# Optimization experiments

Measured on AMD Instinct MI355X. Metric: run time of the kernel, lower is better.

The kernel has to match this reference:

```python
import jax, jax.numpy as jnp
import numpy as np

BN_EPS = 1e-5
K = 3  # k_size


def _unfold(x, k):
    # torch F.unfold with padding=k//2, stride=1, viewed as (B, C, k*k, H, W).
    # Kernel positions are row-major (i slow, j fast), matching torch layout.
    p = k // 2
    B, C, H, W = x.shape
    xp = jnp.pad(x, ((0, 0), (0, 0), (p, p), (p, p)))
    pats = jnp.stack([xp[:, :, i:i + H, j:j + W]
                      for i in range(k) for j in range(k)], axis=2)
    return pats  # (B, C, k*k, H, W)


def _conv1x1(x, w, b):
    # w: (C_out, C_in), x: (B, C_in, H, W)
    return jnp.einsum('oc,bchw->bohw', w, x) + b[None, :, None, None]


def _bn(x, gamma, beta, mean, var):
    inv = gamma / jnp.sqrt(var + BN_EPS)
    return x * inv[None, :, None, None] + (beta - mean * inv)[None, :, None, None]


def setup_inputs() -> dict:
    key = jax.random.key(0)
    ks = jax.random.split(key, 12)
    B, C, H, W = 8, 256, 64, 64
    s = lambda k_, *sh: jax.random.normal(k_, sh, dtype=jnp.float32) * 0.05
    return {
        'x': jax.random.normal(ks[0], (B, C, H, W), dtype=jnp.float32),
        # feature_embedding: Conv2d(C, C, 1) + BN
        'w_embed': s(ks[1], C, C), 'b_embed': jnp.zeros((C,), jnp.float32),
        'bn1_gamma': jnp.ones((C,), jnp.float32), 'bn1_beta': jnp.zeros((C,), jnp.float32),
        'bn1_mean': jnp.zeros((C,), jnp.float32), 'bn1_var': jnp.ones((C,), jnp.float32),
        # enhance: Conv2d(2C, C, 1) + BN
        'w_enh': s(ks[2], C, 2 * C), 'b_enh': jnp.zeros((C,), jnp.float32),
        'bn2_gamma': jnp.ones((C,), jnp.float32), 'bn2_beta': jnp.zeros((C,), jnp.float32),
        'bn2_mean': jnp.zeros((C,), jnp.float32), 'bn2_var': jnp.ones((C,), jnp.float32),
        # weight_gen: Conv2d(2C, C//4, 1) -> ReLU -> Conv2d(C//4, C, 1) -> Sigmoid
        'w_g1': s(ks[3], C // 4, 2 * C), 'b_g1': jnp.zeros((C // 4,), jnp.float32),
        'w_g2': s(ks[4], C, C // 4), 'b_g2': jnp.zeros((C,), jnp.float32),
    }


def reference(x, w_embed, b_embed, bn1_gamma, bn1_beta, bn1_mean, bn1_var,
              w_enh, b_enh, bn2_gamma, bn2_beta, bn2_mean, bn2_var,
              w_g1, b_g1, w_g2, b_g2):
    B, C, H, W = x.shape
    # ---- feature embedding: 1x1 conv + BN (eval) + ReLU
    fe = jax.nn.relu(_bn(_conv1x1(x, w_embed, b_embed),
                         bn1_gamma, bn1_beta, bn1_mean, bn1_var))
    # ---- region similarity: cosine(center pixel, each kxk neighbor) over C
    pats = _unfold(fe, K)                       # (B, C, k2, H, W)
    sim = jnp.einsum('bchw,bckhw->bkhw', fe, pats)
    norm_c = jnp.sqrt(jnp.sum(fe * fe, axis=1))             # (B, H, W)
    norm_p = jnp.sqrt(jnp.sum(pats * pats, axis=1))         # (B, k2, H, W)
    sim = sim / (norm_c[:, None] * norm_p + 1e-7)
    sim = jax.nn.softmax(sim, axis=1)                       # over k2 window
    # ---- dynamic feature aggregation on original x
    xpats = _unfold(x, K)                                   # (B, C, k2, H, W)
    agg = jnp.einsum('bckhw,bkhw->bchw', xpats, sim)
    enhanced = jax.nn.relu(_bn(_conv1x1(jnp.concatenate([x, agg], axis=1), w_enh, b_enh),
                               bn2_gamma, bn2_beta, bn2_mean, bn2_var))
    # ---- output modulation (SE-style gating)
    pooled = jnp.mean(jnp.concatenate([x, enhanced], axis=1), axis=(2, 3), keepdims=True)
    h = jax.nn.relu(_conv1x1(pooled, w_g1, b_g1))
    weights = jax.nn.sigmoid(_conv1x1(h, w_g2, b_g2))       # (B, C, 1, 1)
    return x + weights * enhanced
```

## Files before the change

### kernel.cpp

```cpp
#include <hip/hip_runtime.h>
#include <math.h>

typedef unsigned short u16;
typedef unsigned int   u32;
typedef __attribute__((ext_vector_type(8))) short short8;
typedef __attribute__((ext_vector_type(4))) short s16x4;
typedef __attribute__((ext_vector_type(4))) float f32x4;

#define OFS_XB   0ul
#define OFS_W1B  8388608ul
#define OFS_W2B  8421376ul
#define OFS_B1   8486912ul
#define OFS_B2   8487168ul
#define OFS_POOL 8487424ul
#define OFS_ENH  8491520ul

__device__ __forceinline__ u16 f2bf(float x) {
    union { float f; u32 u; } v; v.f = x;
    u32 r = v.u + 0x7fffu + ((v.u >> 16) & 1u);
    return (u16)(r >> 16);
}
__device__ __forceinline__ float bf2f(u16 h) {
    union { u32 u; float f; } v; v.u = ((u32)h) << 16;
    return v.f;
}
__device__ __forceinline__ void ld_g2l_16(u16* l, const u16* g) {
    __builtin_amdgcn_global_load_lds(
        (const __attribute__((address_space(1))) u32*)g,
        (__attribute__((address_space(3))) u32*)l,
        16, 0, 0);
}

__global__ __launch_bounds__(256) void k_cvt(
    const float* __restrict__ x, u16* __restrict__ xb, float* __restrict__ pool,
    const float* __restrict__ w1, const float* __restrict__ b1,
    const float* __restrict__ g1, const float* __restrict__ be1,
    const float* __restrict__ m1, const float* __restrict__ v1,
    const float* __restrict__ w2, const float* __restrict__ b2,
    const float* __restrict__ g2, const float* __restrict__ be2,
    const float* __restrict__ m2, const float* __restrict__ v2,
    u16* __restrict__ w1b, u16* __restrict__ w2b,
    float* __restrict__ b1f, float* __restrict__ b2f)
{
    __shared__ float tile[64][65];
    const int t = threadIdx.x;
    const int id = blockIdx.x;
    if (id < 1) {
        const float4 z = {0.f, 0.f, 0.f, 0.f};
#pragma unroll
        for (int i = 0; i < 4; ++i) ((float4*)pool)[i * 256 + t] = z;
        return;
    }
    if (id < 771) {
        int idx = (id - 1) * 256 + t;
        if (idx < 65536) {
            int o = idx >> 8;
            float inv = g1[o] * rsqrtf(v1[o] + 1e-5f);
            w1b[idx] = f2bf(w1[idx] * inv);
        } else if (idx < 196608) {
            int j = idx - 65536;
            int o = j >> 9;
            float inv = g2[o] * rsqrtf(v2[o] + 1e-5f);
            w2b[j] = f2bf(w2[j] * inv);
        } else if (idx < 196864) {
            int o = idx - 196608;
            float inv = g1[o] * rsqrtf(v1[o] + 1e-5f);
            b1f[o] = b1[o] * inv + be1[o] - m1[o] * inv;
        } else if (idx < 197120) {
            int o = idx - 196864;
            float inv = g2[o] * rsqrtf(v2[o] + 1e-5f);
            b2f[o] = b2[o] * inv + be2[o] - m2[o] * inv;
        }
        return;
    }
    const int cid = id - 771;
    const int pt = cid & 63, ct = (cid >> 6) & 3, b = cid >> 8;
    const float* src = x + (((size_t)(b * 256 + ct * 64)) << 12) + pt * 64;
#pragma unroll
    for (int i = 0; i < 16; ++i) {
        int idx = i * 256 + t;
        int cl = idx >> 6, pl = idx & 63;
        tile[cl][pl] = src[((size_t)cl << 12) + pl];
    }
    __syncthreads();
#pragma unroll
    for (int i = 0; i < 8; ++i) {
        int idx = i * 256 + t;
        int pl = idx >> 5, c2 = idx & 31;
        int cl = c2 * 2;
        u32 lo = f2bf(tile[cl][pl]);
        u32 hi = f2bf(tile[cl + 1][pl]);
        *(u32*)(xb + (((size_t)(b * 4096 + pt * 64 + pl)) << 9) + ct * 64 + cl) = lo | (hi << 16);
    }
    if (t < 64) {
        float s = 0.f;
#pragma unroll
        for (int i = 0; i < 64; ++i) s += tile[t][i];
        atomicAdd(&pool[(b << 9) + ct * 64 + t], s * (1.f / 4096.f));
    }
}

template<int KIN, bool OUTT, bool DOPOOL>
__global__ __launch_bounds__(256) void k_gemm(
    const u16* __restrict__ xb, const u16* __restrict__ Wb,
    const float* __restrict__ biasf, void* __restrict__ outp,
    float* __restrict__ poolp)
{
    __shared__ __align__(16) u16 Wl[4096];
    __shared__ __align__(16) u16 Xl[4096];
    __shared__ __align__(16) u16 ct[OUTT ? 16384 : 4];
    __shared__ float sbias[128];
    const int t = threadIdx.x;
    const int lane = t & 63;
    const int wv = t >> 6;
    const int id = blockIdx.x;
    const int p_blk = (((id >> 4) << 3) | (id & 7)) * 128;
    const int o_blk = ((id >> 3) & 1) * 128;
    const int owg = (wv & 1) * 4;
    const int pwg = (wv >> 1) * 4;
    const int r16 = lane & 15, q = lane >> 4;
    if (t < 128) sbias[t] = biasf[o_blk + t];

    f32x4 acc[4][4];
#pragma unroll
    for (int i = 0; i < 4; ++i)
#pragma unroll
        for (int j = 0; j < 4; ++j) acc[i][j] = (f32x4){0.f, 0.f, 0.f, 0.f};

    for (int kc = 0; kc < KIN / 32; ++kc) {
        const int kk = kc * 32 + q * 8;
#pragma unroll
        for (int s = 0; s < 4; ++s) {
            const int bi = wv * 4 + s;
            const u16* g;
            u16* l;
            if (bi < 8) {
                g = Wb + (size_t)(o_blk + bi * 16 + r16) * KIN + kk;
                l = Wl + bi * 512;
            } else {
                g = xb + (((size_t)(p_blk + (bi - 8) * 16 + r16)) << 9) + kk;
                l = Xl + (bi - 8) * 512;
            }
            ld_g2l_16(l, g);
        }
        __syncthreads();
        short8 af[4], bf[4];
#pragma unroll
        for (int i = 0; i < 4; ++i) af[i] = *(const short8*)(Wl + (owg + i) * 512 + lane * 8);
#pragma unroll
        for (int j = 0; j < 4; ++j) bf[j] = *(const short8*)(Xl + (pwg + j) * 512 + lane * 8);
#pragma unroll
        for (int i = 0; i < 4; ++i)
#pragma unroll
            for (int j = 0; j < 4; ++j)
                acc[i][j] = __builtin_amdgcn_mfma_f32_16x16x32_bf16(af[i], bf[j], acc[i][j], 0, 0, 0);
        __syncthreads();
    }

    float bia[4][4];
#pragma unroll
    for (int i = 0; i < 4; ++i)
#pragma unroll
        for (int r = 0; r < 4; ++r) bia[i][r] = sbias[owg * 16 + i * 16 + q * 4 + r];
    const int bidx = p_blk >> 12;

    if (OUTT) {
#pragma unroll
        for (int i = 0; i < 4; ++i) {
#pragma unroll
            for (int j = 0; j < 4; ++j) {
                const int px_l = pwg * 16 + j * 16 + r16;
#pragma unroll
                for (int rp = 0; rp < 2; ++rp) {
                    const int r0 = rp * 2;
                    const int o_l = owg * 16 + i * 16 + q * 4 + r0;
                    const float v0 = fmaxf(acc[i][j][r0] + bia[i][r0], 0.f);
                    const float v1 = fmaxf(acc[i][j][r0 + 1] + bia[i][r0 + 1], 0.f);
                    const u32 pk = (u32)f2bf(v0) | ((u32)f2bf(v1) << 16);
                    *(u32*)((char*)ct + px_l * 256 + ((o_l * 2) ^ ((px_l & 7) << 4))) = pk;
                }
            }
        }
        __syncthreads();
        u16* feT = (u16*)outp;
#pragma unroll
        for (int it = 0; it < 16; ++it) {
            const int idx = it * 256 + t;
            const int px_l = idx >> 5, cd = idx & 31;
            s16x4 v = *(const s16x4*)((char*)ct + px_l * 256 + ((cd * 8) ^ ((px_l & 7) << 4)));
            *(s16x4*)(feT + (((size_t)(bidx * 4096 + (p_blk & 4095) + px_l)) << 8) + o_blk + cd * 4) = v;
        }
        return;
    }

    const int pin0 = (p_blk & 4095) + pwg * 16 + r16;
#pragma unroll
    for (int i = 0; i < 4; ++i) {
#pragma unroll
        for (int r = 0; r < 4; ++r) {
            const int o = o_blk + owg * 16 + i * 16 + q * 4 + r;
            const size_t rowb = ((size_t)(bidx * 256 + o)) << 12;
            float ps = 0.f;
#pragma unroll
            for (int j = 0; j < 4; ++j) {
                float v = fmaxf(acc[i][j][r] + bia[i][r], 0.f);
                const size_t oi = rowb + pin0 + j * 16;
                ((u16*)outp)[oi] = f2bf(v);
                ps += v;
            }
            if (DOPOOL) {
                ps += __shfl_down(ps, 8, 16);
                ps += __shfl_down(ps, 4, 16);
                ps += __shfl_down(ps, 2, 16);
                ps += __shfl_down(ps, 1, 16);
                if (r16 == 0)
                    atomicAdd(&poolp[(bidx << 9) + 256 + o], ps * (1.f / 4096.f));
            }
        }
    }
}

__global__ __launch_bounds__(512) void k_simagg(
    const u16* __restrict__ fe, const u16* __restrict__ xb, u16* __restrict__ xbo)
{
    __shared__ float red[8][64][13];
    __shared__ float ws9[9][64];
    const int t = threadIdx.x;
    const int id = blockIdx.x;
    const int b = id & 7, h = id >> 3;
    const int rows[3] = {h > 0 ? h - 1 : 0, h, h < 63 ? h + 1 : 63};
    const int w = t & 63, sl = t >> 6;

    {
        const int wl = w > 0 ? w - 1 : 0, wr = w < 63 ? w + 1 : 63;
        const int pxs[3] = {wl, w, wr};
        const u16* feb = fe + (((size_t)(b * 4096)) << 8) + sl * 32;
        float cvec[32];
        float dot[9];
        float nn0 = 0.f, nn2 = 0.f;
        {
            const u16* p = feb + (((size_t)(rows[1] * 64 + w)) << 8);
            float s = 0.f;
#pragma unroll
            for (int i = 0; i < 4; ++i) {
                short8 v = *(const short8*)(p + i * 8);
#pragma unroll
                for (int u = 0; u < 8; ++u) {
                    float f = bf2f((u16)v[u]);
                    cvec[i * 8 + u] = f;
                    s = fmaf(f, f, s);
                }
            }
            dot[4] = s;
        }
#pragma unroll
        for (int r = 0; r < 3; ++r) {
#pragma unroll
            for (int j = 0; j < 3; ++j) {
                if (r == 1 && j == 1) continue;
                const int k = r * 3 + j;
                const u16* p = feb + (((size_t)(rows[r] * 64 + pxs[j])) << 8);
                float s = 0.f, qq = 0.f;
#pragma unroll
                for (int i = 0; i < 4; ++i) {
                    short8 v = *(const short8*)(p + i * 8);
#pragma unroll
                    for (int u = 0; u < 8; ++u) {
                        float f = bf2f((u16)v[u]);
                        s = fmaf(cvec[i * 8 + u], f, s);
                        if (j == 1) qq = fmaf(f, f, qq);
                    }
                }
                dot[k] = s;
                if (j == 1) { if (r == 0) nn0 = qq; else nn2 = qq; }
            }
        }
#pragma unroll
        for (int k = 0; k < 9; ++k) red[sl][w][k] = dot[k];
        red[sl][w][9] = nn0;
        red[sl][w][10] = nn2;
    }
    __syncthreads();
    if (t < 64) {
        float dk[9];
#pragma unroll
        for (int k = 0; k < 9; ++k) {
            float s = red[0][w][k];
#pragma unroll
            for (int g = 1; g < 8; ++g) s += red[g][w][k];
            dk[k] = s;
        }
        float nr0 = red[0][w][9], nr2 = red[0][w][10];
#pragma unroll
        for (int g = 1; g < 8; ++g) { nr0 += red[g][w][9]; nr2 += red[g][w][10]; }
        float nr[3] = {nr0, dk[4], nr2};
        const float nc = sqrtf(dk[4]);
        float sv[9], mk[9];
#pragma unroll
        for (int di = -1; di <= 1; ++di) {
#pragma unroll
            for (int dj = -1; dj <= 1; ++dj) {
                const int k = (di + 1) * 3 + (dj + 1);
                const int hn = h + di, wn = w + dj;
                const float mask = (hn >= 0 && hn < 64 && wn >= 0 && wn < 64) ? 1.f : 0.f;
                const int wc = wn < 0 ? 0 : (wn > 63 ? 63 : wn);
                const float nk = __shfl(nr[di + 1], wc, 64);
                mk[k] = mask;
                sv[k] = mask * dk[k] / (nc * sqrtf(nk) + 1e-7f);
            }
        }
        float mx = sv[0];
#pragma unroll
        for (int k = 1; k < 9; ++k) mx = fmaxf(mx, sv[k]);
        float e[9], sum = 0.f;
#pragma unroll
        for (int k = 0; k < 9; ++k) { e[k] = expf(sv[k] - mx); sum += e[k]; }
        const float rs = 1.f / sum;
#pragma unroll
        for (int k = 0; k < 9; ++k) ws9[k][w] = mk[k] * e[k] * rs;
    }
    __syncthreads();
    const int cd = t & 63, pxg = t >> 6;
    const u16* xbb = xb + (((size_t)(b * 4096)) << 9) + cd * 4;
    u16* orow = xbo + (((size_t)(b * 4096 + h * 64)) << 9) + 256 + cd * 4;
#pragma unroll
    for (int pi = 0; pi < 8; ++pi) {
        const int px = pxg * 8 + pi;
        const int pL = px > 0 ? px - 1 : 0, pR = px < 63 ? px + 1 : 63;
        const int pxs2[3] = {pL, px, pR};
        float m9[9];
#pragma unroll
        for (int k = 0; k < 9; ++k) m9[k] = ws9[k][px];
        float a0 = 0.f, a1 = 0.f, a2 = 0.f, a3 = 0.f;
#pragma unroll
        for (int r = 0; r < 3; ++r) {
#pragma unroll
            for (int j = 0; j < 3; ++j) {
                const float m = m9[r * 3 + j];
                s16x4 v = *(const s16x4*)(xbb + (((size_t)(rows[r] * 64 + pxs2[j])) << 9));
                a0 = fmaf(bf2f((u16)v[0]), m, a0);
                a1 = fmaf(bf2f((u16)v[1]), m, a1);
                a2 = fmaf(bf2f((u16)v[2]), m, a2);
                a3 = fmaf(bf2f((u16)v[3]), m, a3);
            }
        }
        s16x4 sv4;
        sv4[0] = (short)f2bf(a0); sv4[1] = (short)f2bf(a1);
        sv4[2] = (short)f2bf(a2); sv4[3] = (short)f2bf(a3);
        *(s16x4*)(orow + ((size_t)px << 9)) = sv4;
    }
}

__global__ __launch_bounds__(256) void k_final(
    const float* __restrict__ x, const u16* __restrict__ enh,
    const float* __restrict__ pool,
    const float* __restrict__ wg1, const float* __restrict__ bg1,
    const float* __restrict__ wg2, const float* __restrict__ bg2,
    float* __restrict__ out)
{
    __shared__ float pl[512];
    __shared__ float hpart[4][64];
    __shared__ float hb[64];
    __shared__ float sg[256];
    const int t = threadIdx.x;
    const int id = blockIdx.x;
    const int b = id & 7, cg = id >> 3;
    pl[t] = pool[b * 512 + t];
    pl[t + 256] = pool[b * 512 + 256 + t];
    __syncthreads();
    {
        const int o = t & 63, seg = t >> 6;
        float s = 0.f;
        const float* wr_ = wg1 + o * 512 + seg * 128;
        const float* pr_ = pl + seg * 128;
#pragma unroll 4
        for (int j = 0; j < 128; ++j) s = fmaf(wr_[j], pr_[j], s);
        hpart[seg][o] = s;
    }
    __syncthreads();
    if (t < 64)
        hb[t] = fmaxf(hpart[0][t] + hpart[1][t] + hpart[2][t] + hpart[3][t] + bg1[t], 0.f);
    __syncthreads();
    {
        float s2 = bg2[t];
        const float* w2 = wg2 + t * 64;
#pragma unroll 4
        for (int j = 0; j < 64; ++j) s2 = fmaf(w2[j], hb[j], s2);
        sg[t] = 1.f / (1.f + expf(-s2));
    }
    __syncthreads();
    const int cl = t >> 6, l = t & 63;
    const int c = cg * 4 + cl;
    const float gt = sg[c];
    const float* xp = x + (((size_t)(b * 256 + c)) << 12);
    const u16*   ep = enh + (((size_t)(b * 256 + c)) << 12);
    float*       op = out + (((size_t)(b * 256 + c)) << 12);
#pragma unroll
    for (int ch = 0; ch < 8; ++ch) {
        const int base = ch * 512 + l * 8;
        short8 ev = *(const short8*)(ep + base);
        float4 x0 = *(const float4*)(xp + base);
        float4 x1 = *(const float4*)(xp + base + 4);
        float4 o0, o1;
        o0.x = fmaf(gt, bf2f((u16)ev[0]), x0.x);
        o0.y = fmaf(gt, bf2f((u16)ev[1]), x0.y);
        o0.z = fmaf(gt, bf2f((u16)ev[2]), x0.z);
        o0.w = fmaf(gt, bf2f((u16)ev[3]), x0.w);
        o1.x = fmaf(gt, bf2f((u16)ev[4]), x1.x);
        o1.y = fmaf(gt, bf2f((u16)ev[5]), x1.y);
        o1.z = fmaf(gt, bf2f((u16)ev[6]), x1.z);
        o1.w = fmaf(gt, bf2f((u16)ev[7]), x1.w);
        *(float4*)(op + base) = o0;
        *(float4*)(op + base + 4) = o1;
    }
}

extern "C" void kernel_launch(void* const* d_in, const int* in_sizes, int n_in,
                              void* d_out, int out_size, void* d_ws, size_t ws_size,
                              hipStream_t stream)
{
    const float* x       = (const float*)d_in[0];
    const float* w_embed = (const float*)d_in[1];
    const float* b_embed = (const float*)d_in[2];
    const float* g1      = (const float*)d_in[3];
    const float* be1     = (const float*)d_in[4];
    const float* m1      = (const float*)d_in[5];
    const float* v1      = (const float*)d_in[6];
    const float* w_enh   = (const float*)d_in[7];
    const float* b_enh   = (const float*)d_in[8];
    const float* g2      = (const float*)d_in[9];
    const float* be2     = (const float*)d_in[10];
    const float* m2      = (const float*)d_in[11];
    const float* v2      = (const float*)d_in[12];
    const float* w_g1    = (const float*)d_in[13];
    const float* b_g1    = (const float*)d_in[14];
    const float* w_g2    = (const float*)d_in[15];
    const float* b_g2    = (const float*)d_in[16];
    float* ws  = (float*)d_ws;
    float* out = (float*)d_out;

    u16*   xb   = (u16*)(ws + OFS_XB);
    u16*   w1b  = (u16*)(ws + OFS_W1B);
    u16*   w2b  = (u16*)(ws + OFS_W2B);
    float* b1f  = ws + OFS_B1;
    float* b2f  = ws + OFS_B2;
    float* pool = ws + OFS_POOL;
    u16*   enh  = (u16*)(ws + OFS_ENH);
    u16*   fe   = (u16*)d_out;

    k_cvt<<<dim3(2819), dim3(256), 0, stream>>>(
        x, xb, pool,
        w_embed, b_embed, g1, be1, m1, v1,
        w_enh, b_enh, g2, be2, m2, v2, w1b, w2b, b1f, b2f);
    k_gemm<256, true, false><<<dim3(512), dim3(256), 0, stream>>>(xb, w1b, b1f, (void*)fe, nullptr);
    k_simagg<<<dim3(512), dim3(512), 0, stream>>>(fe, xb, xb);
    k_gemm<512, false, true><<<dim3(512), dim3(256), 0, stream>>>(xb, w2b, b2f, (void*)enh, pool);
    k_final<<<dim3(512), dim3(256), 0, stream>>>(x, enh, pool, w_g1, b_g1, w_g2, b_g2, out);
}
```

Measured before the change: 212.7 us.

## Double-buffer GEMM LDS tiles and reuse sliding-window loads in aggregation

The 1x1-conv GEMM kernel now keeps two LDS buffers for the weight and activation tiles and issues the load of the next K-chunk before running the MFMAs on the current one. This is meant to overlap global-to-LDS traffic with matrix math. The aggregation kernel also keeps a 3x3 sliding window of converted bf16 values in registers, so each step loads only one new column instead of nine gathers. Costs are double the LDS footprint, which may lower occupancy, and more registers in the aggregation kernel. The remainder of the GEMM loop is not shown, so it is unclear whether its trailing barrier still protects the buffer being overwritten.

```diff
diff --git a/kernel.cpp b/kernel.cpp
--- a/kernel.cpp
+++ b/kernel.cpp
@@ -106,8 +106,8 @@
     const float* __restrict__ biasf, void* __restrict__ outp,
     float* __restrict__ poolp)
 {
-    __shared__ __align__(16) u16 Wl[4096];
-    __shared__ __align__(16) u16 Xl[4096];
+    __shared__ __align__(16) u16 Wl[2][4096];
+    __shared__ __align__(16) u16 Xl[2][4096];
     __shared__ __align__(16) u16 ct[OUTT ? 16384 : 4];
     __shared__ float sbias[128];
     const int t = threadIdx.x;
@@ -121,13 +121,9 @@
     const int r16 = lane & 15, q = lane >> 4;
     if (t < 128) sbias[t] = biasf[o_blk + t];
 
-    f32x4 acc[4][4];
-#pragma unroll
-    for (int i = 0; i < 4; ++i)
-#pragma unroll
-        for (int j = 0; j < 4; ++j) acc[i][j] = (f32x4){0.f, 0.f, 0.f, 0.f};
-
-    for (int kc = 0; kc < KIN / 32; ++kc) {
+    constexpr int NT = KIN / 32;
+
+    auto STAGE = [&](int buf, int kc) {
         const int kk = kc * 32 + q * 8;
 #pragma unroll
         for (int s = 0; s < 4; ++s) {
@@ -136,19 +132,31 @@
             u16* l;
             if (bi < 8) {
                 g = Wb + (size_t)(o_blk + bi * 16 + r16) * KIN + kk;
-                l = Wl + bi * 512;
+                l = Wl[buf] + bi * 512;
             } else {
                 g = xb + (((size_t)(p_blk + (bi - 8) * 16 + r16)) << 9) + kk;
-                l = Xl + (bi - 8) * 512;
+                l = Xl[buf] + (bi - 8) * 512;
             }
             ld_g2l_16(l, g);
         }
-        __syncthreads();
+    };
+
+    f32x4 acc[4][4];
+#pragma unroll
+    for (int i = 0; i < 4; ++i)
+#pragma unroll
+        for (int j = 0; j < 4; ++j) acc[i][j] = (f32x4){0.f, 0.f, 0.f, 0.f};
+
+    STAGE(0, 0);
+    __syncthreads();
+    for (int kc = 0; kc < NT; ++kc) {
+        const int cur = kc & 1;
+        if (kc + 1 < NT) STAGE(cur ^ 1, kc + 1);
         short8 af[4], bf[4];
 #pragma unroll
-        for (int i = 0; i < 4; ++i) af[i] = *(const short8*)(Wl + (owg + i) * 512 + lane * 8);
-#pragma unroll
-        for (int j = 0; j < 4; ++j) bf[j] = *(const short8*)(Xl + (pwg + j) * 512 + lane * 8);
+        for (int i = 0; i < 4; ++i) af[i] = *(const short8*)(Wl[cur] + (owg + i) * 512 + lane * 8);
+#pragma unroll
+        for (int j = 0; j < 4; ++j) bf[j] = *(const short8*)(Xl[cur] + (pwg + j) * 512 + lane * 8);
 #pragma unroll
         for (int i = 0; i < 4; ++i)
 #pragma unroll
@@ -323,26 +331,58 @@
     const int cd = t & 63, pxg = t >> 6;
     const u16* xbb = xb + (((size_t)(b * 4096)) << 9) + cd * 4;
     u16* orow = xbo + (((size_t)(b * 4096 + h * 64)) << 9) + 256 + cd * 4;
+    const int px0 = pxg * 8;
+    float wv0[3][4], wv1[3][4], wv2[3][4];
+    {
+        const int pm = px0 > 0 ? px0 - 1 : 0;
+#pragma unroll
+        for (int r = 0; r < 3; ++r) {
+            s16x4 a = *(const s16x4*)(xbb + (((size_t)(rows[r] * 64 + pm)) << 9));
+            s16x4 c = *(const s16x4*)(xbb + (((size_t)(rows[r] * 64 + px0)) << 9));
+            s16x4 d = *(const s16x4*)(xbb + (((size_t)(rows[r] * 64 + px0 + 1)) << 9));
+#pragma unroll
+            for (int u = 0; u < 4; ++u) {
+                wv0[r][u] = bf2f((u16)a[u]);
+                wv1[r][u] = bf2f((u16)c[u]);
+                wv2[r][u] = bf2f((u16)d[u]);
+            }
+        }
+    }
 #pragma unroll
     for (int pi = 0; pi < 8; ++pi) {
-        const int px = pxg * 8 + pi;
-        const int pL = px > 0 ? px - 1 : 0, pR = px < 63 ? px + 1 : 63;
-        const int pxs2[3] = {pL, px, pR};
+        const int px = px0 + pi;
+        if (pi > 0) {
+#pragma unroll
+            for (int r = 0; r < 3; ++r)
+#pragma unroll
+                for (int u = 0; u < 4; ++u) { wv0[r][u] = wv1[r][u]; wv1[r][u] = wv2[r][u]; }
+            if (px < 63) {
+#pragma unroll
+                for (int r = 0; r < 3; ++r) {
+                    s16x4 c = *(const s16x4*)(xbb + (((size_t)(rows[r] * 64 + px + 1)) << 9));
+#pragma unroll
+                    for (int u = 0; u < 4; ++u) wv2[r][u] = bf2f((u16)c[u]);
+                }
+            }
+        }
         float m9[9];
 #pragma unroll
         for (int k = 0; k < 9; ++k) m9[k] = ws9[k][px];
         float a0 = 0.f, a1 = 0.f, a2 = 0.f, a3 = 0.f;
 #pragma unroll
         for (int r = 0; r < 3; ++r) {
-#pragma unroll
-            for (int j = 0; j < 3; ++j) {
-                const float m = m9[r * 3 + j];
-                s16x4 v = *(const s16x4*)(xbb + (((size_t)(rows[r] * 64 + pxs2[j])) << 9));
-                a0 = fmaf(bf2f((u16)v[0]), m, a0);
-                a1 = fmaf(bf2f((u16)v[1]), m, a1);
-                a2 = fmaf(bf2f((u16)v[2]), m, a2);
-                a3 = fmaf(bf2f((u16)v[3]), m, a3);
-            }
+            a0 = fmaf(wv0[r][0], m9[r * 3 + 0], a0);
+            a1 = fmaf(wv0[r][1], m9[r * 3 + 0], a1);
+            a2 = fmaf(wv0[r][2], m9[r * 3 + 0], a2);
+            a3 = fmaf(wv0[r][3], m9[r * 3 + 0], a3);
+            a0 = fmaf(wv1[r][0], m9[r * 3 + 1], a0);
+            a1 = fmaf(wv1[r][1], m9[r * 3 + 1], a1);
+            a2 = fmaf(wv1[r][2], m9[r * 3 + 1], a2);
+            a3 = fmaf(wv1[r][3], m9[r * 3 + 1], a3);
+            a0 = fmaf(wv2[r][0], m9[r * 3 + 2], a0);
+            a1 = fmaf(wv2[r][1], m9[r * 3 + 2], a1);
+            a2 = fmaf(wv2[r][2], m9[r * 3 + 2], a2);
+            a3 = fmaf(wv2[r][3], m9[r * 3 + 2], a3);
         }
         s16x4 sv4;
         sv4[0] = (short)f2bf(a0); sv4[1] = (short)f2bf(a1);
```

Result: no change. 214.0 us (+0.6%).

## Fuse enhance GEMM with SE gating via cooperative grid sync; double-buffer LDS

Applied to the files above, without the earlier changes.

The second GEMM now keeps its accumulators in registers, atomically pools channel means, and performs a grid-wide cooperative sync. It then computes the SE gate and writes the final gated residual output directly, so the separate final kernel and the bf16 enhanced intermediate round trip are gone. Both GEMMs also double-buffer LDS tiles, issuing the next K-slice loads before computing the current one. The trade-offs: the cooperative launch requires all 512 blocks to be co-resident at 2 blocks per CU, and output stores are now narrower, less vectorised fp32 writes.

```diff
diff --git a/kernel.cpp b/kernel.cpp
--- a/kernel.cpp
+++ b/kernel.cpp
@@ -1,5 +1,8 @@
 #include <hip/hip_runtime.h>
+#include <hip/hip_cooperative_groups.h>
 #include <math.h>
+
+namespace cg = cooperative_groups;
 
 typedef unsigned short u16;
 typedef unsigned int   u32;
@@ -13,7 +16,6 @@
 #define OFS_B1   8486912ul
 #define OFS_B2   8487168ul
 #define OFS_POOL 8487424ul
-#define OFS_ENH  8491520ul
 
 __device__ __forceinline__ u16 f2bf(float x) {
     union { float f; u32 u; } v; v.f = x;
@@ -100,15 +102,14 @@
     }
 }
 
-template<int KIN, bool OUTT, bool DOPOOL>
-__global__ __launch_bounds__(256) void k_gemm(
+__global__ __launch_bounds__(256) void k_gemm1(
     const u16* __restrict__ xb, const u16* __restrict__ Wb,
-    const float* __restrict__ biasf, void* __restrict__ outp,
-    float* __restrict__ poolp)
+    const float* __restrict__ biasf, u16* __restrict__ feT)
 {
-    __shared__ __align__(16) u16 Wl[4096];
-    __shared__ __align__(16) u16 Xl[4096];
-    __shared__ __align__(16) u16 ct[OUTT ? 16384 : 4];
+    constexpr int KIN = 256;
+    __shared__ __align__(16) u16 Wl[2][4096];
+    __shared__ __align__(16) u16 Xl[2][4096];
+    __shared__ __align__(16) u16 ct[16384];
     __shared__ float sbias[128];
     const int t = threadIdx.x;
     const int lane = t & 63;
@@ -121,13 +122,8 @@
     const int r16 = lane & 15, q = lane >> 4;
     if (t < 128) sbias[t] = biasf[o_blk + t];
 
-    f32x4 acc[4][4];
-#pragma unroll
-    for (int i = 0; i < 4; ++i)
-#pragma unroll
-        for (int j = 0; j < 4; ++j) acc[i][j] = (f32x4){0.f, 0.f, 0.f, 0.f};
-
-    for (int kc = 0; kc < KIN / 32; ++kc) {
+    constexpr int NT = KIN / 32;
+    auto STAGE = [&](int buf, int kc) {
         const int kk = kc * 32 + q * 8;
 #pragma unroll
         for (int s = 0; s < 4; ++s) {
@@ -136,19 +132,31 @@
             u16* l;
             if (bi < 8) {
                 g = Wb + (size_t)(o_blk + bi * 16 + r16) * KIN + kk;
-                l = Wl + bi * 512;
+                l = Wl[buf] + bi * 512;
             } else {
                 g = xb + (((size_t)(p_blk + (bi - 8) * 16 + r16)) << 9) + kk;
-                l = Xl + (bi - 8) * 512;
+                l = Xl[buf] + (bi - 8) * 512;
             }
             ld_g2l_16(l, g);
         }
-        __syncthreads();
+    };
+
+    f32x4 acc[4][4];
+#pragma unroll
+    for (int i = 0; i < 4; ++i)
+#pragma unroll
+        for (int j = 0; j < 4; ++j) acc[i][j] = (f32x4){0.f, 0.f, 0.f, 0.f};
+
+    STAGE(0, 0);
+    __syncthreads();
+    for (int kc = 0; kc < NT; ++kc) {
+        const int cur = kc & 1;
+        if (kc + 1 < NT) STAGE(cur ^ 1, kc + 1);
         short8 af[4], bf[4];
 #pragma unroll
-        for (int i = 0; i < 4; ++i) af[i] = *(const short8*)(Wl + (owg + i) * 512 + lane * 8);
-#pragma unroll
-        for (int j = 0; j < 4; ++j) bf[j] = *(const short8*)(Xl + (pwg + j) * 512 + lane * 8);
+        for (int i = 0; i < 4; ++i) af[i] = *(const short8*)(Wl[cur] + (owg + i) * 512 + lane * 8);
+#pragma unroll
+        for (int j = 0; j < 4; ++j) bf[j] = *(const short8*)(Xl[cur] + (pwg + j) * 512 + lane * 8);
 #pragma unroll
         for (int i = 0; i < 4; ++i)
 #pragma unroll
@@ -164,59 +172,29 @@
         for (int r = 0; r < 4; ++r) bia[i][r] = sbias[owg * 16 + i * 16 + q * 4 + r];
     const int bidx = p_blk >> 12;
 
-    if (OUTT) {
-#pragma unroll
-        for (int i = 0; i < 4; ++i) {
-#pragma unroll
-            for (int j = 0; j < 4; ++j) {
-                const int px_l = pwg * 16 + j * 16 + r16;
-#pragma unroll
-                for (int rp = 0; rp < 2; ++rp) {
-                    const int r0 = rp * 2;
-                    const int o_l = owg * 16 + i * 16 + q * 4 + r0;
-                    const float v0 = fmaxf(acc[i][j][r0] + bia[i][r0], 0.f);
-                    const float v1 = fmaxf(acc[i][j][r0 + 1] + bia[i][r0 + 1], 0.f);
-                    const u32 pk = (u32)f2bf(v0) | ((u32)f2bf(v1) << 16);
-                    *(u32*)((char*)ct + px_l * 256 + ((o_l * 2) ^ ((px_l & 7) << 4))) = pk;
-                }
-            }
-        }
-        __syncthreads();
-        u16* feT = (u16*)outp;
-#pragma unroll
-        for (int it = 0; it < 16; ++it) {
-            const int idx = it * 256 + t;
-            const int px_l = idx >> 5, cd = idx & 31;
-            s16x4 v = *(const s16x4*)((char*)ct + px_l * 256 + ((cd * 8) ^ ((px_l & 7) << 4)));
-            *(s16x4*)(feT + (((size_t)(bidx * 4096 + (p_blk & 4095) + px_l)) << 8) + o_blk + cd * 4) = v;
-        }
-        return;
-    }
-
-    const int pin0 = (p_blk & 4095) + pwg * 16 + r16;
 #pragma unroll
     for (int i = 0; i < 4; ++i) {
 #pragma unroll
-        for (int r = 0; r < 4; ++r) {
-            const int o = o_blk + owg * 16 + i * 16 + q * 4 + r;
-            const size_t rowb = ((size_t)(bidx * 256 + o)) << 12;
-            float ps = 0.f;
-#pragma unroll
-            for (int j = 0; j < 4; ++j) {
-                float v = fmaxf(acc[i][j][r] + bia[i][r], 0.f);
-                const size_t oi = rowb + pin0 + j * 16;
-                ((u16*)outp)[oi] = f2bf(v);
-                ps += v;
-            }
-            if (DOPOOL) {
-                ps += __shfl_down(ps, 8, 16);
-                ps += __shfl_down(ps, 4, 16);
-                ps += __shfl_down(ps, 2, 16);
-                ps += __shfl_down(ps, 1, 16);
-                if (r16 == 0)
-                    atomicAdd(&poolp[(bidx << 9) + 256 + o], ps * (1.f / 4096.f));
-            }
-        }
+        for (int j = 0; j < 4; ++j) {
+            const int px_l = pwg * 16 + j * 16 + r16;
+#pragma unroll
+            for (int rp = 0; rp < 2; ++rp) {
+                const int r0 = rp * 2;
+                const int o_l = owg * 16 + i * 16 + q * 4 + r0;
+                const float v0 = fmaxf(acc[i][j][r0] + bia[i][r0], 0.f);
+                const float v1 = fmaxf(acc[i][j][r0 + 1] + bia[i][r0 + 1], 0.f);
+                const u32 pk = (u32)f2bf(v0) | ((u32)f2bf(v1) << 16);
+                *(u32*)((char*)ct + px_l * 256 + ((o_l * 2) ^ ((px_l & 7) << 4))) = pk;
+            }
+        }
+    }
+    __syncthreads();
+#pragma unroll
+    for (int it = 0; it < 16; ++it) {
+        const int idx = it * 256 + t;
+        const int px_l = idx >> 5, cd = idx & 31;
+        s16x4 v = *(const s16x4*)((char*)ct + px_l * 256 + ((cd * 8) ^ ((px_l & 7) << 4)));
+        *(s16x4*)(feT + (((size_t)(bidx * 4096 + (p_blk & 4095) + px_l)) << 8) + o_blk + cd * 4) = v;
     }
 }
 
@@ -351,22 +329,104 @@
     }
 }
 
-__global__ __launch_bounds__(256) void k_final(
-    const float* __restrict__ x, const u16* __restrict__ enh,
-    const float* __restrict__ pool,
+__global__ __launch_bounds__(256, 2) void k_gemm2f(
+    const u16* __restrict__ xb, const u16* __restrict__ Wb,
+    const float* __restrict__ biasf, const float* __restrict__ x,
     const float* __restrict__ wg1, const float* __restrict__ bg1,
     const float* __restrict__ wg2, const float* __restrict__ bg2,
-    float* __restrict__ out)
+    float* __restrict__ pool, float* __restrict__ out)
 {
+    constexpr int KIN = 512;
+    __shared__ __align__(16) u16 Wl[2][4096];
+    __shared__ __align__(16) u16 Xl[2][4096];
+    __shared__ float sbias[128];
     __shared__ float pl[512];
     __shared__ float hpart[4][64];
     __shared__ float hb[64];
     __shared__ float sg[256];
     const int t = threadIdx.x;
+    const int lane = t & 63;
+    const int wv = t >> 6;
     const int id = blockIdx.x;
-    const int b = id & 7, cg = id >> 3;
-    pl[t] = pool[b * 512 + t];
-    pl[t + 256] = pool[b * 512 + 256 + t];
+    const int p_blk = (((id >> 4) << 3) | (id & 7)) * 128;
+    const int o_blk = ((id >> 3) & 1) * 128;
+    const int owg = (wv & 1) * 4;
+    const int pwg = (wv >> 1) * 4;
+    const int r16 = lane & 15, q = lane >> 4;
+    if (t < 128) sbias[t] = biasf[o_blk + t];
+
+    constexpr int NT = KIN / 32;
+    auto STAGE = [&](int buf, int kc) {
+        const int kk = kc * 32 + q * 8;
+#pragma unroll
+        for (int s = 0; s < 4; ++s) {
+            const int bi = wv * 4 + s;
+            const u16* g;
+            u16* l;
+            if (bi < 8) {
+                g = Wb + (size_t)(o_blk + bi * 16 + r16) * KIN + kk;
+                l = Wl[buf] + bi * 512;
+            } else {
+                g = xb + (((size_t)(p_blk + (bi - 8) * 16 + r16)) << 9) + kk;
+                l = Xl[buf] + (bi - 8) * 512;
+            }
+            ld_g2l_16(l, g);
+        }
+    };
+
+    f32x4 acc[4][4];
+#pragma unroll
+    for (int i = 0; i < 4; ++i)
+#pragma unroll
+        for (int j = 0; j < 4; ++j) acc[i][j] = (f32x4){0.f, 0.f, 0.f, 0.f};
+
+    STAGE(0, 0);
+    __syncthreads();
+    for (int kc = 0; kc < NT; ++kc) {
+        const int cur = kc & 1;
+        if (kc + 1 < NT) STAGE(cur ^ 1, kc + 1);
+        short8 af[4], bf[4];
+#pragma unroll
+        for (int i = 0; i < 4; ++i) af[i] = *(const short8*)(Wl[cur] + (owg + i) * 512 + lane * 8);
+#pragma unroll
+        for (int j = 0; j < 4; ++j) bf[j] = *(const short8*)(Xl[cur] + (pwg + j) * 512 + lane * 8);
+#pragma unroll
+        for (int i = 0; i < 4; ++i)
+#pragma unroll
+            for (int j = 0; j < 4; ++j)
+                acc[i][j] = __builtin_amdgcn_mfma_f32_16x16x32_bf16(af[i], bf[j], acc[i][j], 0, 0, 0);
+        __syncthreads();
+    }
+
+    float bia[4][4];
+#pragma unroll
+    for (int i = 0; i < 4; ++i)
+#pragma unroll
+        for (int r = 0; r < 4; ++r) bia[i][r] = sbias[owg * 16 + i * 16 + q * 4 + r];
+    const int bidx = p_blk >> 12;
+
+#pragma unroll
+    for (int i = 0; i < 4; ++i) {
+#pragma unroll
+        for (int r = 0; r < 4; ++r) {
+            const int o = o_blk + owg * 16 + i * 16 + q * 4 + r;
+            float ps = 0.f;
+#pragma unroll
+            for (int j = 0; j < 4; ++j)
+                ps += fmaxf(acc[i][j][r] + bia[i][r], 0.f);
+            ps += __shfl_down(ps, 8, 16);
+            ps += __shfl_down(ps, 4, 16);
+            ps += __shfl_down(ps, 2, 16);
+            ps += __shfl_down(ps, 1, 16);
+            if (r16 == 0)
+                atomicAdd(&pool[(bidx << 9) + 256 + o], ps * (1.f / 4096.f));
+        }
+    }
+    __threadfence();
+    cg::this_grid().sync();
+
+    pl[t] = pool[bidx * 512 + t];
+    pl[t + 256] = pool[bidx * 512 + 256 + t];
     __syncthreads();
     {
         const int o = t & 63, seg = t >> 6;
@@ -389,29 +449,22 @@
         sg[t] = 1.f / (1.f + expf(-s2));
     }
     __syncthreads();
-    const int cl = t >> 6, l = t & 63;
-    const int c = cg * 4 + cl;
-    const float gt = sg[c];
-    const float* xp = x + (((size_t)(b * 256 + c)) << 12);
-    const u16*   ep = enh + (((size_t)(b * 256 + c)) << 12);
-    float*       op = out + (((size_t)(b * 256 + c)) << 12);
-#pragma unroll
-    for (int ch = 0; ch < 8; ++ch) {
-        const int base = ch * 512 + l * 8;
-        short8 ev = *(const short8*)(ep + base);
-        float4 x0 = *(const float4*)(xp + base);
-        float4 x1 = *(const float4*)(xp + base + 4);
-        float4 o0, o1;
-        o0.x = fmaf(gt, bf2f((u16)ev[0]), x0.x);
-        o0.y = fmaf(gt, bf2f((u16)ev[1]), x0.y);
-        o0.z = fmaf(gt, bf2f((u16)ev[2]), x0.z);
-        o0.w = fmaf(gt, bf2f((u16)ev[3]), x0.w);
-        o1.x = fmaf(gt, bf2f((u16)ev[4]), x1.x);
-        o1.y = fmaf(gt, bf2f((u16)ev[5]), x1.y);
-        o1.z = fmaf(gt, bf2f((u16)ev[6]), x1.z);
-        o1.w = fmaf(gt, bf2f((u16)ev[7]), x1.w);
-        *(float4*)(op + base) = o0;
-        *(float4*)(op + base + 4) = o1;
+
+    const int pin0 = (p_blk & 4095) + pwg * 16 + r16;
+#pragma unroll
+    for (int i = 0; i < 4; ++i) {
+#pragma unroll
+        for (int r = 0; r < 4; ++r) {
+            const int o = o_blk + owg * 16 + i * 16 + q * 4 + r;
+            const float gt = sg[o];
+            const size_t rowb = ((size_t)(bidx * 256 + o)) << 12;
+#pragma unroll
+            for (int j = 0; j < 4; ++j) {
+                const float v = fmaxf(acc[i][j][r] + bia[i][r], 0.f);
+                const size_t off = rowb + pin0 + j * 16;
+                out[off] = fmaf(gt, v, x[off]);
+            }
+        }
     }
 }
 
@@ -445,15 +498,19 @@
     float* b1f  = ws + OFS_B1;
     float* b2f  = ws + OFS_B2;
     float* pool = ws + OFS_POOL;
-    u16*   enh  = (u16*)(ws + OFS_ENH);
     u16*   fe   = (u16*)d_out;
 
     k_cvt<<<dim3(2819), dim3(256), 0, stream>>>(
         x, xb, pool,
         w_embed, b_embed, g1, be1, m1, v1,
         w_enh, b_enh, g2, be2, m2, v2, w1b, w2b, b1f, b2f);
-    k_gemm<256, true, false><<<dim3(512), dim3(256), 0, stream>>>(xb, w1b, b1f, (void*)fe, nullptr);
+    k_gemm1<<<dim3(512), dim3(256), 0, stream>>>(xb, w1b, b1f, fe);
     k_simagg<<<dim3(512), dim3(512), 0, stream>>>(fe, xb, xb);
-    k_gemm<512, false, true><<<dim3(512), dim3(256), 0, stream>>>(xb, w2b, b2f, (void*)enh, pool);
-    k_final<<<dim3(512), dim3(256), 0, stream>>>(x, enh, pool, w_g1, b_g1, w_g2, b_g2, out);
-}
+    {
+        void* args[] = {(void*)&xb, (void*)&w2b, (void*)&b2f, (void*)&x,
+                        (void*)&w_g1, (void*)&b_g1, (void*)&w_g2, (void*)&b_g2,
+                        (void*)&pool, (void*)&out};
+        hipLaunchCooperativeKernel((const void*)k_gemm2f, dim3(512), dim3(256),
+                                   args, 0, stream);
+    }
+}
```

After: 315.5 us. 48.4% more time.
